# Kernel tuning notes

Hardware: AMD Instinct MI355X
Metric: run time of the kernel (lower is better)

Reference implementation:

```python
import jax, jax.numpy as jnp
import numpy as np

N_ATOMS = 200_000
N_PAIRS = 8_000_000
N_CH = 4
EXPONENT = 1.0  # p in 1/r^p potential


def setup_inputs() -> dict:
    key = jax.random.key(0)
    k1, k2, k3 = jax.random.split(key, 3)
    charges = jax.random.normal(k1, (N_ATOMS, N_CH), dtype=jnp.float32)
    neighbor_indices = jax.random.randint(k2, (N_PAIRS, 2), 0, N_ATOMS, dtype=jnp.int32)
    # distances within a physical cutoff shell, bounded away from 0 to keep 1/r^p finite
    neighbor_distances = jax.random.uniform(k3, (N_PAIRS,), dtype=jnp.float32, minval=0.5, maxval=5.0)
    return {
        "charges": charges,
        "neighbor_indices": neighbor_indices,
        "neighbor_distances": neighbor_distances,
    }


def reference(charges, neighbor_indices, neighbor_distances):
    # non-periodic path: potentials_bare = InversePowerLawPotential.from_dist(r) = 1/r^p
    potentials_bare = neighbor_distances ** (-EXPONENT)  # [n_pairs]
    atom_is = neighbor_indices[:, 0]
    atom_js = neighbor_indices[:, 1]
    w = potentials_bare[:, None]  # [n_pairs, 1]
    contributions_is = charges[atom_js] * w  # gather j-charges, scale by pair potential
    contributions_js = charges[atom_is] * w  # gather i-charges (half neighbor list symmetrization)
    potential = jnp.zeros_like(charges)
    potential = potential.at[atom_is].add(contributions_is)
    potential = potential.at[atom_js].add(contributions_js)  # use_half_neighborlist=True
    return potential / 2
```

## Files before the change

kernel.cpp:

```cpp
#include <hip/hip_runtime.h>
#include <hip/hip_fp16.h>


#define BLOCK 1024
#define NSLICES 10
#define CT_BLOCK 256
#define SC_BLOCK 256
#define SC_PPT 8
#define CA_BITS 12
#define NCHUNK 49
#define PLANE_PAD 16
#define FB_NSL 10
#define FB_UNROLL 8

__device__ __forceinline__ void fadd(float* p, float v) {
#if defined(__HIP_DEVICE_COMPILE__)
    unsafeAtomicAdd(p, v);
#else
    atomicAdd(p, v);
#endif
}

__device__ __forceinline__ void pkadd(__half2* p, float lo, float hi) {
#if defined(__HIP_DEVICE_COMPILE__)
    __half2 v = __float22half2_rn(make_float2(lo, hi));
    unsigned bits;
    __builtin_memcpy(&bits, &v, 4);
    unsigned off = (unsigned)(unsigned long long)(void*)p;
    asm volatile("ds_pk_add_f16 %0, %1" :: "v"(off), "v"(bits) : "memory");
#else
    (void)p; (void)lo; (void)hi;
#endif
}

__global__ __launch_bounds__(CT_BLOCK) void bucket_count(
    const int4* __restrict__ idx2, unsigned* __restrict__ counts, int npairs)
{
    __shared__ unsigned hist[NCHUNK * 4];
    for (int b = threadIdx.x; b < NCHUNK * 4; b += CT_BLOCK) hist[b] = 0;
    __syncthreads();
    const int n4 = npairs >> 1;
    const int r = threadIdx.x & 3;
    const int stride = gridDim.x * CT_BLOCK;
    for (int q = blockIdx.x * CT_BLOCK + threadIdx.x; q < n4; q += stride) {
        int4 v = idx2[q];
        atomicAdd(&hist[(((unsigned)v.x >> CA_BITS) << 2) + r], 1u);
        atomicAdd(&hist[(((unsigned)v.y >> CA_BITS) << 2) + r], 1u);
        atomicAdd(&hist[(((unsigned)v.z >> CA_BITS) << 2) + r], 1u);
        atomicAdd(&hist[(((unsigned)v.w >> CA_BITS) << 2) + r], 1u);
    }
    if ((npairs & 1) && blockIdx.x == 0 && threadIdx.x == 0) {
        const int2* idx = (const int2*)idx2;
        int2 ij = idx[npairs - 1];
        atomicAdd(&counts[(unsigned)ij.x >> CA_BITS], 1u);
        atomicAdd(&counts[(unsigned)ij.y >> CA_BITS], 1u);
    }
    __syncthreads();
    for (int b = threadIdx.x; b < NCHUNK; b += CT_BLOCK) {
        unsigned t = hist[4 * b] + hist[4 * b + 1] + hist[4 * b + 2] + hist[4 * b + 3];
        if (t) atomicAdd(&counts[b], t);
    }
}

__global__ void bucket_prefix(const unsigned* __restrict__ counts,
                              unsigned* __restrict__ offsets,
                              unsigned* __restrict__ cursors, int nbuckets)
{
    if (threadIdx.x == 0 && blockIdx.x == 0) {
        unsigned acc = 0;
        for (int b = 0; b < nbuckets; ++b) {
            offsets[b] = acc; cursors[b] = acc; acc += counts[b];
        }
        offsets[nbuckets] = acc;
    }
}

__global__ __launch_bounds__(SC_BLOCK) void bucket_scatter(
    const int2*  __restrict__ idx, const float* __restrict__ dist,
    uint2* __restrict__ entries, unsigned* __restrict__ cursors, int npairs)
{
    __shared__ unsigned hist[NCHUNK * 4];
    __shared__ unsigned rbase[NCHUNK * 4];
    for (int b = threadIdx.x; b < NCHUNK * 4; b += SC_BLOCK) hist[b] = 0;
    __syncthreads();

    const int p0 = blockIdx.x * (SC_BLOCK * SC_PPT) + threadIdx.x;
    const unsigned r = threadIdx.x & 3;
    unsigned key[2 * SC_PPT];
    unsigned brk[2 * SC_PPT];
    float    wv[SC_PPT];

#pragma unroll
    for (int k = 0; k < SC_PPT; ++k) {
        int p = p0 + k * SC_BLOCK;
        if (p < npairs) {
            int2 ij = idx[p];
            wv[k] = 0.5f / dist[p];
            unsigned s0 = (((unsigned)ij.x >> CA_BITS) << 2) + r;
            unsigned s1 = (((unsigned)ij.y >> CA_BITS) << 2) + r;
            key[2 * k]     = (unsigned)ij.y | (((unsigned)ij.x & ((1u << CA_BITS) - 1)) << 18);
            brk[2 * k]     = s0 | (atomicAdd(&hist[s0], 1u) << 8);
            key[2 * k + 1] = (unsigned)ij.x | (((unsigned)ij.y & ((1u << CA_BITS) - 1)) << 18);
            brk[2 * k + 1] = s1 | (atomicAdd(&hist[s1], 1u) << 8);
        } else {
            brk[2 * k] = brk[2 * k + 1] = 0xFFFFFFFFu;
        }
    }
    __syncthreads();
    if (threadIdx.x < NCHUNK) {
        int b = threadIdx.x;
        unsigned h0 = hist[4 * b], h1 = hist[4 * b + 1], h2 = hist[4 * b + 2], h3 = hist[4 * b + 3];
        unsigned tot = h0 + h1 + h2 + h3;
        unsigned g = tot ? atomicAdd(&cursors[b], tot) : 0u;
        rbase[4 * b]     = g;
        rbase[4 * b + 1] = g + h0;
        rbase[4 * b + 2] = g + h0 + h1;
        rbase[4 * b + 3] = g + h0 + h1 + h2;
    }
    __syncthreads();

#pragma unroll
    for (int k = 0; k < SC_PPT; ++k) {
        if (brk[2 * k] != 0xFFFFFFFFu) {
            unsigned wb = __float_as_uint(wv[k]);
            entries[rbase[brk[2 * k] & 255u] + (brk[2 * k] >> 8)] =
                make_uint2(key[2 * k], wb);
            entries[rbase[brk[2 * k + 1] & 255u] + (brk[2 * k + 1] >> 8)] =
                make_uint2(key[2 * k + 1], wb);
        }
    }
}

template<int CHUNK_ATOMS>
__global__ __launch_bounds__(BLOCK) void bucket_scan(
    const float4* __restrict__ charges, const uint2* __restrict__ entries,
    const unsigned* __restrict__ offsets, float* __restrict__ slabs,
    int natoms)
{
    constexpr int PLANE = CHUNK_ATOMS + PLANE_PAD;
    extern __shared__ __half2 sm2[];
    __half2* smp0 = sm2;
    __half2* smp1 = sm2 + PLANE;

    const int c  = blockIdx.x / NSLICES;
    const int s  = blockIdx.x - c * NSLICES;
    {
        unsigned* z = (unsigned*)sm2;
        for (int e = threadIdx.x; e < 2 * PLANE; e += BLOCK) z[e] = 0u;
    }
    __syncthreads();

    const unsigned beg = offsets[c];
    const unsigned cnt = offsets[c + 1] - beg;
    const unsigned e0  = beg + (unsigned)((unsigned long long)cnt * s       / NSLICES);
    const unsigned e1  = beg + (unsigned)((unsigned long long)cnt * (s + 1) / NSLICES);

    auto process = [&](uint2 en) {
        float4 cq = charges[en.x & 0x3FFFFu];
        float w = __uint_as_float(en.y);
        unsigned d = en.x >> 18;
        pkadd(smp0 + d, cq.x * w, cq.y * w);
        pkadd(smp1 + d, cq.z * w, cq.w * w);
    };

    const unsigned e0a = min(e1, (e0 + 1u) & ~1u);
    for (unsigned e = e0 + threadIdx.x; e < e0a; e += BLOCK) process(entries[e]);

    const uint4* ent4 = (const uint4*)entries;
    const unsigned base = e0a >> 1;
    const unsigned n4   = (e1 - e0a) >> 1;
    const unsigned nb   = n4 / (BLOCK * 4);

    unsigned q = base + threadIdx.x;
    for (unsigned b = 0; b < nb; ++b, q += BLOCK * 4) {
        uint4 E[4];
#pragma unroll
        for (int u = 0; u < 4; ++u) E[u] = ent4[q + u * BLOCK];
        float4 cq[8];
#pragma unroll
        for (int u = 0; u < 4; ++u) {
            cq[2 * u]     = charges[E[u].x & 0x3FFFFu];
            cq[2 * u + 1] = charges[E[u].z & 0x3FFFFu];
        }
#pragma unroll
        for (int u = 0; u < 4; ++u) {
            float w0 = __uint_as_float(E[u].y);
            unsigned d0 = E[u].x >> 18;
            pkadd(smp0 + d0, cq[2 * u].x * w0, cq[2 * u].y * w0);
            pkadd(smp1 + d0, cq[2 * u].z * w0, cq[2 * u].w * w0);
            float w1 = __uint_as_float(E[u].w);
            unsigned d1 = E[u].z >> 18;
            pkadd(smp0 + d1, cq[2 * u + 1].x * w1, cq[2 * u + 1].y * w1);
            pkadd(smp1 + d1, cq[2 * u + 1].z * w1, cq[2 * u + 1].w * w1);
        }
    }
    for (unsigned q2 = base + nb * (BLOCK * 4) + threadIdx.x; q2 < base + n4; q2 += BLOCK) {
        uint4 E = ent4[q2];
        process(make_uint2(E.x, E.y));
        process(make_uint2(E.z, E.w));
    }
    for (unsigned e = e0a + 2 * n4 + threadIdx.x; e < e1; e += BLOCK) process(entries[e]);
    __syncthreads();

    const int c0 = c * CHUNK_ATOMS;
    const int cn = min(CHUNK_ATOMS, natoms - c0);
    float4* dst = (float4*)(slabs + (size_t)blockIdx.x * (CHUNK_ATOMS * 4));
    for (int a = threadIdx.x; a < cn; a += BLOCK) {
        float2 f01 = __half22float2(smp0[a]);
        float2 f23 = __half22float2(smp1[a]);
        dst[a] = make_float4(f01.x, f01.y, f23.x, f23.y);
    }
}

template<int CH_ELEMS, int NS>
__global__ __launch_bounds__(256) void chunk_reduce(
    const float4* __restrict__ ws, float4* __restrict__ out, int total4)
{
    int g = blockIdx.x * blockDim.x + threadIdx.x;
    if (g >= total4) return;
    constexpr int CH4 = CH_ELEMS / 4;
    int c = g / CH4;
    int local = g - c * CH4;
    const float4* p = ws + ((size_t)c * NS) * CH4 + local;
    float4 acc = make_float4(0.f, 0.f, 0.f, 0.f);
#pragma unroll
    for (int s = 0; s < NS; ++s) {
        float4 v = p[(size_t)s * CH4];
        acc.x += v.x; acc.y += v.y; acc.z += v.z; acc.w += v.w;
    }
    out[g] = acc;
}

template<int CHUNK_ATOMS, bool USE_WS>
__global__ __launch_bounds__(BLOCK) void chunk_scan(
    const float4* __restrict__ charges, const int2* __restrict__ idx,
    const float* __restrict__ dist, float* __restrict__ dest,
    int npairs, int natoms)
{
    constexpr int CH_ELEMS = CHUNK_ATOMS * 4;
    extern __shared__ float sm[];
    const int c  = blockIdx.x / FB_NSL;
    const int s  = blockIdx.x - c * FB_NSL;
    const int c0 = c * CHUNK_ATOMS;
    const int cn = min(CHUNK_ATOMS, natoms - c0);
    for (int e = threadIdx.x; e < CH_ELEMS; e += BLOCK) sm[e] = 0.f;
    __syncthreads();
    const int p0 = (int)((long long)npairs * s       / FB_NSL);
    const int p1 = (int)((long long)npairs * (s + 1) / FB_NSL);
    const int nbatch = (p1 - p0) / (BLOCK * FB_UNROLL);
    int p = p0 + threadIdx.x;
    for (int b = 0; b < nbatch; ++b, p += BLOCK * FB_UNROLL) {
        int2 ij[FB_UNROLL]; float dd[FB_UNROLL];
#pragma unroll
        for (int u = 0; u < FB_UNROLL; ++u) { ij[u] = idx[p + u * BLOCK]; dd[u] = dist[p + u * BLOCK]; }
#pragma unroll
        for (int u = 0; u < FB_UNROLL; ++u) {
            unsigned li = (unsigned)(ij[u].x - c0), lj = (unsigned)(ij[u].y - c0);
            float w = 0.5f / dd[u];
            if (li < (unsigned)cn) {
                float4 cq = charges[ij[u].y]; float* bp = sm + li * 4;
                fadd(bp + 0, cq.x * w); fadd(bp + 1, cq.y * w);
                fadd(bp + 2, cq.z * w); fadd(bp + 3, cq.w * w);
            }
            if (lj < (unsigned)cn) {
                float4 cq = charges[ij[u].x]; float* bp = sm + lj * 4;
                fadd(bp + 0, cq.x * w); fadd(bp + 1, cq.y * w);
                fadd(bp + 2, cq.z * w); fadd(bp + 3, cq.w * w);
            }
        }
    }
    for (; p < p1; p += BLOCK) {
        int2 ij = idx[p];
        unsigned li = (unsigned)(ij.x - c0), lj = (unsigned)(ij.y - c0);
        if (li < (unsigned)cn || lj < (unsigned)cn) {
            float w = 0.5f / dist[p];
            if (li < (unsigned)cn) {
                float4 cq = charges[ij.y]; float* bp = sm + li * 4;
                fadd(bp + 0, cq.x * w); fadd(bp + 1, cq.y * w);
                fadd(bp + 2, cq.z * w); fadd(bp + 3, cq.w * w);
            }
            if (lj < (unsigned)cn) {
                float4 cq = charges[ij.x]; float* bp = sm + lj * 4;
                fadd(bp + 0, cq.x * w); fadd(bp + 1, cq.y * w);
                fadd(bp + 2, cq.z * w); fadd(bp + 3, cq.w * w);
            }
        }
    }
    __syncthreads();
    const int nvalid = cn * 4;
    if (USE_WS) {
        float* dst = dest + (size_t)blockIdx.x * CH_ELEMS;
        for (int e = threadIdx.x; e < nvalid; e += BLOCK) dst[e] = sm[e];
    } else {
        float* dst = dest + (size_t)c0 * 4;
        for (int e = threadIdx.x; e < nvalid; e += BLOCK) fadd(dst + e, sm[e]);
    }
}

extern "C" void kernel_launch(void* const* d_in, const int* in_sizes, int n_in,
                              void* d_out, int out_size, void* d_ws, size_t ws_size,
                              hipStream_t stream) {
    const float4* charges = (const float4*)d_in[0];
    const int2*   idx     = (const int2*)  d_in[1];
    const float*  dist    = (const float*) d_in[2];
    float*        out     = (float*)d_out;

    const int natoms = in_sizes[0] / 4;
    const int npairs = in_sizes[2];
    const int total  = out_size;

    int dev = 0;
    hipGetDevice(&dev);
    int maxShm = 0;
    hipDeviceGetAttribute(&maxShm, hipDeviceAttributeMaxSharedMemoryPerBlock, dev);
    const bool big = (maxShm >= 65536);

    constexpr int CA = 4096, CE = CA * 4;
    const int C    = (natoms + CA - 1) / CA;
    const int grid = C * NSLICES;
    const size_t scan_shm = (size_t)2 * (CA + PLANE_PAD) * sizeof(__half2);

    const size_t ENT_OFF    = 1024;
    const size_t ent_bytes  = (size_t)2 * npairs * sizeof(uint2);
    size_t slab_off         = (ENT_OFF + ent_bytes + 255) & ~(size_t)255;
    const size_t slab_bytes = (size_t)grid * CE * sizeof(float);
    const size_t need       = slab_off + slab_bytes;

    if (big && ws_size >= need && natoms <= (1 << 18) && C == NCHUNK && (total & 3) == 0) {
        unsigned* counts  = (unsigned*)d_ws;
        unsigned* offsets = (unsigned*)((char*)d_ws + 256);
        unsigned* cursors = (unsigned*)((char*)d_ws + 512);
        uint2*    entries = (uint2*)((char*)d_ws + ENT_OFF);
        float*    slabs   = (float*)((char*)d_ws + slab_off);

        hipMemsetAsync(d_ws, 0, 1024, stream);
        bucket_count<<<1024, CT_BLOCK, 0, stream>>>((const int4*)idx, counts, npairs);
        bucket_prefix<<<1, 32, 0, stream>>>(counts, offsets, cursors, C);
        const int sc_grid = (npairs + SC_BLOCK * SC_PPT - 1) / (SC_BLOCK * SC_PPT);
        bucket_scatter<<<sc_grid, SC_BLOCK, 0, stream>>>(idx, dist, entries, cursors, npairs);
        hipFuncSetAttribute((const void*)bucket_scan<CA>,
                            hipFuncAttributeMaxDynamicSharedMemorySize, (int)scan_shm);
        bucket_scan<CA><<<grid, BLOCK, scan_shm, stream>>>(charges, entries, offsets, slabs, natoms);
        chunk_reduce<CE, NSLICES><<<(total / 4 + 255) / 256, 256, 0, stream>>>(
            (const float4*)slabs, (float4*)out, total / 4);
    } else if (big) {
        const size_t ws_need = (size_t)grid * CE * sizeof(float);
        if (ws_size >= ws_need && (total & 3) == 0) {
            hipFuncSetAttribute((const void*)chunk_scan<CA, true>,
                                hipFuncAttributeMaxDynamicSharedMemorySize, CE * 4);
            chunk_scan<CA, true><<<grid, BLOCK, CE * 4, stream>>>(
                charges, idx, dist, (float*)d_ws, npairs, natoms);
            chunk_reduce<CE, FB_NSL><<<(total / 4 + 255) / 256, 256, 0, stream>>>(
                (const float4*)d_ws, (float4*)out, total / 4);
        } else {
            hipMemsetAsync(d_out, 0, (size_t)total * sizeof(float), stream);
            hipFuncSetAttribute((const void*)chunk_scan<CA, false>,
                                hipFuncAttributeMaxDynamicSharedMemorySize, CE * 4);
            chunk_scan<CA, false><<<grid, BLOCK, CE * 4, stream>>>(
                charges, idx, dist, out, npairs, natoms);
        }
    } else {
        constexpr int CA2 = 2048, CE2 = CA2 * 4;
        const int C2 = (natoms + CA2 - 1) / CA2;
        const int grid2 = C2 * FB_NSL;
        const size_t ws_need = (size_t)grid2 * CE2 * sizeof(float);
        if (ws_size >= ws_need && (total & 3) == 0) {
            chunk_scan<CA2, true><<<grid2, BLOCK, CE2 * 4, stream>>>(
                charges, idx, dist, (float*)d_ws, npairs, natoms);
            chunk_reduce<CE2, FB_NSL><<<(total / 4 + 255) / 256, 256, 0, stream>>>(
                (const float4*)d_ws, (float4*)out, total / 4);
        } else {
            hipMemsetAsync(d_out, 0, (size_t)total * sizeof(float), stream);
            chunk_scan<CA2, false><<<grid2, BLOCK, CE2 * 4, stream>>>(
                charges, idx, dist, out, npairs, natoms);
        }
    }
}
```

Before: 436.2 us.

## Store partial slabs in fp16 and use per-thread private histograms for bucket counting

The bucket_scan kernel now writes its per-slice partial sums as raw half2 pairs instead of widening them to float4, which halves slab write traffic. A new chunk_reduce_h kernel reads those halves, converts them to float and accumulates. bucket_count replaces shared-memory atomics with per-thread private histograms that are summed at the end. This costs a larger shared footprint (about 50 KB per block), which may lower occupancy, and a serial 256-step reduction per bucket.

```diff
diff --git a/kernel.cpp b/kernel.cpp
--- a/kernel.cpp
+++ b/kernel.cpp
@@ -36,29 +36,34 @@
 __global__ __launch_bounds__(CT_BLOCK) void bucket_count(
     const int4* __restrict__ idx2, unsigned* __restrict__ counts, int npairs)
 {
-    __shared__ unsigned hist[NCHUNK * 4];
-    for (int b = threadIdx.x; b < NCHUNK * 4; b += CT_BLOCK) hist[b] = 0;
-    __syncthreads();
+    __shared__ unsigned ph[CT_BLOCK * NCHUNK];
+    unsigned* mine = ph + threadIdx.x * NCHUNK;
+#pragma unroll
+    for (int b = 0; b < NCHUNK; ++b) mine[b] = 0;
+    __syncthreads();
+
     const int n4 = npairs >> 1;
-    const int r = threadIdx.x & 3;
     const int stride = gridDim.x * CT_BLOCK;
     for (int q = blockIdx.x * CT_BLOCK + threadIdx.x; q < n4; q += stride) {
         int4 v = idx2[q];
-        atomicAdd(&hist[(((unsigned)v.x >> CA_BITS) << 2) + r], 1u);
-        atomicAdd(&hist[(((unsigned)v.y >> CA_BITS) << 2) + r], 1u);
-        atomicAdd(&hist[(((unsigned)v.z >> CA_BITS) << 2) + r], 1u);
-        atomicAdd(&hist[(((unsigned)v.w >> CA_BITS) << 2) + r], 1u);
+        ++mine[(unsigned)v.x >> CA_BITS];
+        ++mine[(unsigned)v.y >> CA_BITS];
+        ++mine[(unsigned)v.z >> CA_BITS];
+        ++mine[(unsigned)v.w >> CA_BITS];
     }
     if ((npairs & 1) && blockIdx.x == 0 && threadIdx.x == 0) {
         const int2* idx = (const int2*)idx2;
         int2 ij = idx[npairs - 1];
-        atomicAdd(&counts[(unsigned)ij.x >> CA_BITS], 1u);
-        atomicAdd(&counts[(unsigned)ij.y >> CA_BITS], 1u);
-    }
-    __syncthreads();
+        ++mine[(unsigned)ij.x >> CA_BITS];
+        ++mine[(unsigned)ij.y >> CA_BITS];
+    }
+    __syncthreads();
+
     for (int b = threadIdx.x; b < NCHUNK; b += CT_BLOCK) {
-        unsigned t = hist[4 * b] + hist[4 * b + 1] + hist[4 * b + 2] + hist[4 * b + 3];
-        if (t) atomicAdd(&counts[b], t);
+        unsigned s = 0;
+#pragma unroll 8
+        for (int t = 0; t < CT_BLOCK; ++t) s += ph[t * NCHUNK + b];
+        if (s) atomicAdd(&counts[b], s);
     }
 }
 
@@ -134,7 +139,7 @@
 template<int CHUNK_ATOMS>
 __global__ __launch_bounds__(BLOCK) void bucket_scan(
     const float4* __restrict__ charges, const uint2* __restrict__ entries,
-    const unsigned* __restrict__ offsets, float* __restrict__ slabs,
+    const unsigned* __restrict__ offsets, uint2* __restrict__ slabs,
     int natoms)
 {
     constexpr int PLANE = CHUNK_ATOMS + PLANE_PAD;
@@ -204,12 +209,36 @@
 
     const int c0 = c * CHUNK_ATOMS;
     const int cn = min(CHUNK_ATOMS, natoms - c0);
-    float4* dst = (float4*)(slabs + (size_t)blockIdx.x * (CHUNK_ATOMS * 4));
+    uint2* dst = slabs + (size_t)blockIdx.x * CHUNK_ATOMS;
     for (int a = threadIdx.x; a < cn; a += BLOCK) {
-        float2 f01 = __half22float2(smp0[a]);
-        float2 f23 = __half22float2(smp1[a]);
-        dst[a] = make_float4(f01.x, f01.y, f23.x, f23.y);
-    }
+        unsigned b0, b1;
+        __builtin_memcpy(&b0, &smp0[a], 4);
+        __builtin_memcpy(&b1, &smp1[a], 4);
+        dst[a] = make_uint2(b0, b1);
+    }
+}
+
+template<int CH_ATOMS, int NS>
+__global__ __launch_bounds__(256) void chunk_reduce_h(
+    const uint2* __restrict__ ws, float4* __restrict__ out, int natoms_total)
+{
+    int g = blockIdx.x * blockDim.x + threadIdx.x;
+    if (g >= natoms_total) return;
+    int c = g / CH_ATOMS;
+    int local = g - c * CH_ATOMS;
+    const uint2* p = ws + ((size_t)c * NS) * CH_ATOMS + local;
+    float4 acc = make_float4(0.f, 0.f, 0.f, 0.f);
+#pragma unroll
+    for (int s = 0; s < NS; ++s) {
+        uint2 v = p[(size_t)s * CH_ATOMS];
+        __half2 h01, h23;
+        __builtin_memcpy(&h01, &v.x, 4);
+        __builtin_memcpy(&h23, &v.y, 4);
+        float2 f01 = __half22float2(h01);
+        float2 f23 = __half22float2(h23);
+        acc.x += f01.x; acc.y += f01.y; acc.z += f23.x; acc.w += f23.y;
+    }
+    out[g] = acc;
 }
 
 template<int CH_ELEMS, int NS>
@@ -320,29 +349,33 @@
     const int grid = C * NSLICES;
     const size_t scan_shm = (size_t)2 * (CA + PLANE_PAD) * sizeof(__half2);
 
-    const size_t ENT_OFF    = 1024;
-    const size_t ent_bytes  = (size_t)2 * npairs * sizeof(uint2);
-    size_t slab_off         = (ENT_OFF + ent_bytes + 255) & ~(size_t)255;
-    const size_t slab_bytes = (size_t)grid * CE * sizeof(float);
-    const size_t need       = slab_off + slab_bytes;
-
-    if (big && ws_size >= need && natoms <= (1 << 18) && C == NCHUNK && (total & 3) == 0) {
+    const size_t ENT_OFF     = 1024;
+    const size_t ent_bytes   = (size_t)2 * npairs * sizeof(uint2);
+    const size_t slab_off    = (ENT_OFF + ent_bytes + 255) & ~(size_t)255;
+    const size_t slabh_bytes = (size_t)grid * CA * sizeof(uint2);
+    const bool shape_ok = big && natoms <= (1 << 18) && C == NCHUNK
+                          && (total & 3) == 0 && total == 4 * natoms;
+    const bool main_ok = shape_ok && ws_size >= slab_off + slabh_bytes;
+
+    if (main_ok) {
         unsigned* counts  = (unsigned*)d_ws;
         unsigned* offsets = (unsigned*)((char*)d_ws + 256);
         unsigned* cursors = (unsigned*)((char*)d_ws + 512);
         uint2*    entries = (uint2*)((char*)d_ws + ENT_OFF);
-        float*    slabs   = (float*)((char*)d_ws + slab_off);
+        uint2*    slabs   = (uint2*)((char*)d_ws + slab_off);
 
         hipMemsetAsync(d_ws, 0, 1024, stream);
         bucket_count<<<1024, CT_BLOCK, 0, stream>>>((const int4*)idx, counts, npairs);
         bucket_prefix<<<1, 32, 0, stream>>>(counts, offsets, cursors, C);
         const int sc_grid = (npairs + SC_BLOCK * SC_PPT - 1) / (SC_BLOCK * SC_PPT);
-        bucket_scatter<<<sc_grid, SC_BLOCK, 0, stream>>>(idx, dist, entries, cursors, npairs);
+        bucket_scatter<<<sc_grid, SC_BLOCK, 0, stream>>>(
+            idx, dist, entries, cursors, npairs);
         hipFuncSetAttribute((const void*)bucket_scan<CA>,
                             hipFuncAttributeMaxDynamicSharedMemorySize, (int)scan_shm);
-        bucket_scan<CA><<<grid, BLOCK, scan_shm, stream>>>(charges, entries, offsets, slabs, natoms);
-        chunk_reduce<CE, NSLICES><<<(total / 4 + 255) / 256, 256, 0, stream>>>(
-            (const float4*)slabs, (float4*)out, total / 4);
+        bucket_scan<CA><<<grid, BLOCK, scan_shm, stream>>>(
+            charges, entries, offsets, slabs, natoms);
+        chunk_reduce_h<CA, NSLICES><<<(natoms + 255) / 256, 256, 0, stream>>>(
+            slabs, (float4*)out, natoms);
     } else if (big) {
         const size_t ws_need = (size_t)grid * CE * sizeof(float);
         if (ws_size >= ws_need && (total & 3) == 0) {
```

Result: no change. 440.4 us (+0.9%).
